# Optimization experiments

Hardware: AMD Instinct MI355X
Metric: run time of the kernel (lower is better)

## Reference

```python
import jax, jax.numpy as jnp
import numpy as np

N_NODES = 50000
N_EDGES = 300000
D_NODE = 128
D_EDGE = 128
D_HID = 256
D_OUT = 128


def setup_inputs() -> dict:
    key = jax.random.key(0)
    k1, k2, k3, k4, k5, k6, k7 = jax.random.split(key, 7)
    node_attr = jax.random.normal(k1, (N_NODES, D_NODE), dtype=jnp.float32)
    edge_contact_attr = jax.random.normal(k2, (N_EDGES, D_EDGE), dtype=jnp.float32)
    edge_contact_index = jax.random.randint(k3, (2, N_EDGES), 0, N_NODES, dtype=jnp.int32)
    d_in = 2 * D_NODE + D_EDGE  # 384: [sender, receiver, edge] concat
    W1 = jax.random.normal(k4, (d_in, D_HID), dtype=jnp.float32) / jnp.sqrt(jnp.float32(d_in))
    b1 = jnp.zeros((D_HID,), dtype=jnp.float32)
    W2 = jax.random.normal(k5, (D_HID, D_OUT), dtype=jnp.float32) / jnp.sqrt(jnp.float32(D_HID))
    b2 = jnp.zeros((D_OUT,), dtype=jnp.float32)
    ln_gamma = jnp.ones((D_OUT,), dtype=jnp.float32)
    ln_beta = jnp.zeros((D_OUT,), dtype=jnp.float32)
    return {
        "node_attr": node_attr,
        "edge_contact_attr": edge_contact_attr,
        "edge_contact_index": edge_contact_index,
        "W1": W1, "b1": b1, "W2": W2, "b2": b2,
        "ln_gamma": ln_gamma, "ln_beta": ln_beta,
    }


def _layer_norm(x, gamma, beta, eps=1e-5):
    mu = jnp.mean(x, axis=-1, keepdims=True)
    var = jnp.var(x, axis=-1, keepdims=True)
    return (x - mu) * jax.lax.rsqrt(var + eps) * gamma + beta


def reference(node_attr, edge_contact_attr, edge_contact_index,
              W1, b1, W2, b2, ln_gamma, ln_beta):
    senders_idx = edge_contact_index[0]
    receivers_idx = edge_contact_index[1]
    senders_attr = node_attr[senders_idx]      # [E, D_NODE] gather
    receivers_attr = node_attr[receivers_idx]  # [E, D_NODE] gather
    edge_messages = jnp.concatenate(
        [senders_attr, receivers_attr, edge_contact_attr], axis=1)  # [E, 384]
    h = jax.nn.relu(edge_messages @ W1 + b1)   # [E, D_HID]
    h = h @ W2 + b2                            # [E, D_OUT]
    new_edge_contact_attr = _layer_norm(h, ln_gamma, ln_beta)
    return new_edge_contact_attr
```

## Files before the change

### kernel.cpp

```cpp
#include <hip/hip_runtime.h>

#define E_TOT   300000
#define DN      128
#define DOUT    128

typedef float  f32x4  __attribute__((ext_vector_type(4)));
typedef __bf16 bf16x8 __attribute__((ext_vector_type(8)));

__device__ __forceinline__ unsigned short f2bf(float f) {
    union { float f; unsigned int u; } v; v.f = f;
    return (unsigned short)((v.u + 0x7FFFu + ((v.u >> 16) & 1u)) >> 16);
}

__global__ void prep_weights(const float* __restrict__ W1,
                             const float* __restrict__ W2,
                             unsigned short* __restrict__ W1p,
                             unsigned short* __restrict__ W2p) {
    int t = blockIdx.x * 256 + threadIdx.x;
    if (t < 384 * 256) {
        int k = t >> 8, n = t & 255;
        W1p[(((k >> 6) << 8) + n) * 64 + (k & 63)] = f2bf(W1[t]);
    } else {
        int t2 = t - 384 * 256;
        int k = t2 >> 7, n = t2 & 127;
        W2p[(((k >> 6) << 7) + n) * 64 + (k & 63)] = f2bf(W2[t2]);
    }
}

__global__ __launch_bounds__(256, 3) void edge_mlp(
    const float* __restrict__ node_attr,
    const float* __restrict__ edge_attr,
    const int*   __restrict__ eidx,
    const unsigned short* __restrict__ W1p,
    const unsigned short* __restrict__ W2p,
    const float* __restrict__ b1,
    const float* __restrict__ b2,
    const float* __restrict__ ln_g,
    const float* __restrict__ ln_b,
    float* __restrict__ out)
{
    __shared__ __align__(16) unsigned short smem[26112];
    __shared__ int sIdx[64], rIdx[64];

    unsigned short* Xc   = smem;
    unsigned short* W1c  = smem + 4608;
    unsigned short* hbuf = smem;
    unsigned short* W2c  = smem + 16896;

    const int tid  = threadIdx.x;
    const int wid  = tid >> 6;
    const int lane = tid & 63;
    const int quad = lane >> 4;
    const int l16  = lane & 15;
    const int eb   = blockIdx.x * 64;

    if (tid < 128) {
        int r = tid & 63;
        int e = eb + r; if (e >= E_TOT) e = E_TOT - 1;
        if (tid < 64) sIdx[r] = eidx[e];
        else          rIdx[r] = eidx[E_TOT + e];
    }

    f32x4 acc[4][4];
    #pragma unroll
    for (int i = 0; i < 4; ++i)
        #pragma unroll
        for (int j = 0; j < 4; ++j)
            acc[i][j] = (f32x4){0.f, 0.f, 0.f, 0.f};

    __syncthreads();

    #pragma unroll 1
    for (int c = 0; c < 6; ++c) {
        if (c) __syncthreads();
        const int coloff = (c & 1) << 6;
        #pragma unroll
        for (int i = 0; i < 4; ++i) {
            int id  = (i << 8) + tid;
            int row = id >> 4;
            int q4  = id & 15;
            const float* src;
            if (c < 2)      src = node_attr + (size_t)sIdx[row] * DN;
            else if (c < 4) src = node_attr + (size_t)rIdx[row] * DN;
            else {
                int e = eb + row; if (e >= E_TOT) e = E_TOT - 1;
                src = edge_attr + (size_t)e * DN;
            }
            float4 v = *(const float4*)(src + coloff + (q4 << 2));
            ushort4 p;
            p.x = f2bf(v.x); p.y = f2bf(v.y); p.z = f2bf(v.z); p.w = f2bf(v.w);
            *(ushort4*)(Xc + row * 72 + (q4 << 2)) = p;
        }
        const unsigned short* wsrc = W1p + c * (256 * 64);
        #pragma unroll
        for (int i = 0; i < 8; ++i) {
            int id = (i << 8) + tid;
            *(uint4*)(W1c + (id >> 3) * 72 + ((id & 7) << 3)) =
                *(const uint4*)(wsrc + (id << 3));
        }
        __syncthreads();
        #pragma unroll
        for (int ks = 0; ks < 2; ++ks) {
            bf16x8 a[4];
            #pragma unroll
            for (int mt = 0; mt < 4; ++mt)
                a[mt] = *(const bf16x8*)(Xc + ((mt << 4) + l16) * 72 + (ks << 5) + (quad << 3));
            #pragma unroll
            for (int nt = 0; nt < 4; ++nt) {
                bf16x8 b = *(const bf16x8*)(W1c + ((wid << 6) + (nt << 4) + l16) * 72 + (ks << 5) + (quad << 3));
                #pragma unroll
                for (int mt = 0; mt < 4; ++mt)
                    acc[mt][nt] = __builtin_amdgcn_mfma_f32_16x16x32_bf16(a[mt], b, acc[mt][nt], 0, 0, 0);
            }
        }
    }

    float b1v[4];
    #pragma unroll
    for (int nt = 0; nt < 4; ++nt) b1v[nt] = b1[(wid << 6) + (nt << 4) + l16];
    __syncthreads();
    #pragma unroll
    for (int mt = 0; mt < 4; ++mt)
        #pragma unroll
        for (int nt = 0; nt < 4; ++nt)
            #pragma unroll
            for (int r = 0; r < 4; ++r) {
                int row = (mt << 4) + (quad << 2) + r;
                int col = (wid << 6) + (nt << 4) + l16;
                float v = acc[mt][nt][r] + b1v[nt];
                hbuf[row * 264 + col] = f2bf(v > 0.f ? v : 0.f);
            }
    __syncthreads();

    f32x4 acc2[8];
    #pragma unroll
    for (int nt = 0; nt < 8; ++nt) acc2[nt] = (f32x4){0.f, 0.f, 0.f, 0.f};

    #pragma unroll 1
    for (int c2 = 0; c2 < 4; ++c2) {
        if (c2) __syncthreads();
        const unsigned short* wsrc = W2p + c2 * (128 * 64);
        #pragma unroll
        for (int i = 0; i < 4; ++i) {
            int id = (i << 8) + tid;
            *(uint4*)(W2c + (id >> 3) * 72 + ((id & 7) << 3)) =
                *(const uint4*)(wsrc + (id << 3));
        }
        __syncthreads();
        #pragma unroll
        for (int ks = 0; ks < 2; ++ks) {
            bf16x8 a = *(const bf16x8*)(hbuf + ((wid << 4) + l16) * 264 + (c2 << 6) + (ks << 5) + (quad << 3));
            #pragma unroll
            for (int nt = 0; nt < 8; ++nt) {
                bf16x8 b = *(const bf16x8*)(W2c + ((nt << 4) + l16) * 72 + (ks << 5) + (quad << 3));
                acc2[nt] = __builtin_amdgcn_mfma_f32_16x16x32_bf16(a, b, acc2[nt], 0, 0, 0);
            }
        }
    }

    float b2v[8], gv[8], bev[8];
    #pragma unroll
    for (int nt = 0; nt < 8; ++nt) {
        int n = (nt << 4) + l16;
        b2v[nt] = b2[n]; gv[nt] = ln_g[n]; bev[nt] = ln_b[n];
    }
    #pragma unroll
    for (int r = 0; r < 4; ++r) {
        int e = eb + (wid << 4) + (quad << 2) + r;
        float x[8];
        float s = 0.f, s2 = 0.f;
        #pragma unroll
        for (int nt = 0; nt < 8; ++nt) {
            x[nt] = acc2[nt][r] + b2v[nt];
            s += x[nt]; s2 += x[nt] * x[nt];
        }
        #pragma unroll
        for (int m = 1; m < 16; m <<= 1) {
            s  += __shfl_xor(s, m, 64);
            s2 += __shfl_xor(s2, m, 64);
        }
        const float mu  = s * (1.f / 128.f);
        const float var = s2 * (1.f / 128.f) - mu * mu;
        const float rs  = rsqrtf(var + 1e-5f);
        if (e < E_TOT) {
            float* orow = out + (size_t)e * DOUT;
            #pragma unroll
            for (int nt = 0; nt < 8; ++nt)
                orow[(nt << 4) + l16] = (x[nt] - mu) * rs * gv[nt] + bev[nt];
        }
    }
}

extern "C" void kernel_launch(void* const* d_in, const int* in_sizes, int n_in,
                              void* d_out, int out_size, void* d_ws, size_t ws_size,
                              hipStream_t stream) {
    const float* node_attr = (const float*)d_in[0];
    const float* edge_attr = (const float*)d_in[1];
    const int*   eidx      = (const int*)d_in[2];
    const float* W1        = (const float*)d_in[3];
    const float* b1        = (const float*)d_in[4];
    const float* W2        = (const float*)d_in[5];
    const float* b2        = (const float*)d_in[6];
    const float* ln_g      = (const float*)d_in[7];
    const float* ln_b      = (const float*)d_in[8];

    unsigned short* W1p = (unsigned short*)d_ws;
    unsigned short* W2p = W1p + 384 * 256;

    prep_weights<<<512, 256, 0, stream>>>(W1, W2, W1p, W2p);

    const int nblocks = (E_TOT + 63) / 64;
    edge_mlp<<<nblocks, 256, 0, stream>>>(node_attr, edge_attr, eidx,
                                          W1p, W2p, b1, b2, ln_g, ln_b,
                                          (float*)d_out);
}
```

Measured before the change: 418.2 us.

## Load MFMA fragments directly from global memory, bypassing LDS staging

Gathered node and edge features are now loaded from global memory straight into per-lane registers in MFMA A-fragment layout and converted with the packed bf16 conversion instruction. W1 and W2 fragments are also read directly from the pre-packed global buffers instead of being staged through shared memory. This removes most LDS traffic and the per-chunk barriers, and shrinks shared memory to the hidden buffer, which may allow higher occupancy. In exchange each wave re-reads weight data from global/L2 independently, and the activation loads are less coalesced (32-byte pieces per lane).

```diff
diff --git a/kernel.cpp b/kernel.cpp
--- a/kernel.cpp
+++ b/kernel.cpp
@@ -6,10 +6,26 @@
 
 typedef float  f32x4  __attribute__((ext_vector_type(4)));
 typedef __bf16 bf16x8 __attribute__((ext_vector_type(8)));
+typedef unsigned int u32;
 
 __device__ __forceinline__ unsigned short f2bf(float f) {
     union { float f; unsigned int u; } v; v.f = f;
     return (unsigned short)((v.u + 0x7FFFu + ((v.u >> 16) & 1u)) >> 16);
+}
+
+__device__ __forceinline__ u32 cvt_pk_bf16(float lo, float hi) {
+    u32 r;
+    asm("v_cvt_pk_bf16_f32 %0, %1, %2" : "=v"(r) : "v"(lo), "v"(hi));
+    return r;
+}
+
+__device__ __forceinline__ bf16x8 make_frag(float4 u0, float4 u1) {
+    union { u32 w[4]; bf16x8 v; } r;
+    r.w[0] = cvt_pk_bf16(u0.x, u0.y);
+    r.w[1] = cvt_pk_bf16(u0.z, u0.w);
+    r.w[2] = cvt_pk_bf16(u1.x, u1.y);
+    r.w[3] = cvt_pk_bf16(u1.z, u1.w);
+    return r.v;
 }
 
 __global__ void prep_weights(const float* __restrict__ W1,
@@ -39,13 +55,7 @@
     const float* __restrict__ ln_b,
     float* __restrict__ out)
 {
-    __shared__ __align__(16) unsigned short smem[26112];
-    __shared__ int sIdx[64], rIdx[64];
-
-    unsigned short* Xc   = smem;
-    unsigned short* W1c  = smem + 4608;
-    unsigned short* hbuf = smem;
-    unsigned short* W2c  = smem + 16896;
+    __shared__ __align__(16) unsigned short hbuf[64 * 264];
 
     const int tid  = threadIdx.x;
     const int wid  = tid >> 6;
@@ -54,11 +64,14 @@
     const int l16  = lane & 15;
     const int eb   = blockIdx.x * 64;
 
-    if (tid < 128) {
-        int r = tid & 63;
-        int e = eb + r; if (e >= E_TOT) e = E_TOT - 1;
-        if (tid < 64) sIdx[r] = eidx[e];
-        else          rIdx[r] = eidx[E_TOT + e];
+    u32 offS[4], offR[4], offE[4];
+    #pragma unroll
+    for (int mt = 0; mt < 4; ++mt) {
+        int e = eb + (mt << 4) + l16;
+        if (e >= E_TOT) e = E_TOT - 1;
+        offS[mt] = (u32)eidx[e] * (DN * 4);
+        offR[mt] = (u32)eidx[E_TOT + e] * (DN * 4);
+        offE[mt] = (u32)e * (DN * 4);
     }
 
     f32x4 acc[4][4];
@@ -68,49 +81,33 @@
         for (int j = 0; j < 4; ++j)
             acc[i][j] = (f32x4){0.f, 0.f, 0.f, 0.f};
 
-    __syncthreads();
-
+    const int fbase = ((0) << 6);
+    (void)fbase;
     #pragma unroll 1
     for (int c = 0; c < 6; ++c) {
-        if (c) __syncthreads();
-        const int coloff = (c & 1) << 6;
-        #pragma unroll
-        for (int i = 0; i < 4; ++i) {
-            int id  = (i << 8) + tid;
-            int row = id >> 4;
-            int q4  = id & 15;
-            const float* src;
-            if (c < 2)      src = node_attr + (size_t)sIdx[row] * DN;
-            else if (c < 4) src = node_attr + (size_t)rIdx[row] * DN;
-            else {
-                int e = eb + row; if (e >= E_TOT) e = E_TOT - 1;
-                src = edge_attr + (size_t)e * DN;
-            }
-            float4 v = *(const float4*)(src + coloff + (q4 << 2));
-            ushort4 p;
-            p.x = f2bf(v.x); p.y = f2bf(v.y); p.z = f2bf(v.z); p.w = f2bf(v.w);
-            *(ushort4*)(Xc + row * 72 + (q4 << 2)) = p;
-        }
-        const unsigned short* wsrc = W1p + c * (256 * 64);
-        #pragma unroll
-        for (int i = 0; i < 8; ++i) {
-            int id = (i << 8) + tid;
-            *(uint4*)(W1c + (id >> 3) * 72 + ((id & 7) << 3)) =
-                *(const uint4*)(wsrc + (id << 3));
-        }
-        __syncthreads();
+        const int f0 = ((c & 1) << 6) + (quad << 3);
+        bf16x8 a[2][4];
+        #pragma unroll
+        for (int mt = 0; mt < 4; ++mt) {
+            u32 off = (c < 2) ? offS[mt] : (c < 4) ? offR[mt] : offE[mt];
+            const char* basep = (const char*)((c < 4) ? node_attr : edge_attr);
+            const float* s = (const float*)(basep + off);
+            float4 u0 = *(const float4*)(s + f0);
+            float4 u1 = *(const float4*)(s + f0 + 4);
+            float4 v0 = *(const float4*)(s + f0 + 32);
+            float4 v1 = *(const float4*)(s + f0 + 36);
+            a[0][mt] = make_frag(u0, u1);
+            a[1][mt] = make_frag(v0, v1);
+        }
+        const unsigned short* wbase = W1p + (((c << 8) + (wid << 6)) << 6);
         #pragma unroll
         for (int ks = 0; ks < 2; ++ks) {
-            bf16x8 a[4];
-            #pragma unroll
-            for (int mt = 0; mt < 4; ++mt)
-                a[mt] = *(const bf16x8*)(Xc + ((mt << 4) + l16) * 72 + (ks << 5) + (quad << 3));
             #pragma unroll
             for (int nt = 0; nt < 4; ++nt) {
-                bf16x8 b = *(const bf16x8*)(W1c + ((wid << 6) + (nt << 4) + l16) * 72 + (ks << 5) + (quad << 3));
+                bf16x8 b = *(const bf16x8*)(wbase + (((nt << 4) + l16) << 6) + (ks << 5) + (quad << 3));
                 #pragma unroll
                 for (int mt = 0; mt < 4; ++mt)
-                    acc[mt][nt] = __builtin_amdgcn_mfma_f32_16x16x32_bf16(a[mt], b, acc[mt][nt], 0, 0, 0);
+                    acc[mt][nt] = __builtin_amdgcn_mfma_f32_16x16x32_bf16(a[ks][mt], b, acc[mt][nt], 0, 0, 0);
             }
         }
     }
@@ -118,7 +115,6 @@
     float b1v[4];
     #pragma unroll
     for (int nt = 0; nt < 4; ++nt) b1v[nt] = b1[(wid << 6) + (nt << 4) + l16];
-    __syncthreads();
     #pragma unroll
     for (int mt = 0; mt < 4; ++mt)
         #pragma unroll
@@ -138,21 +134,13 @@
 
     #pragma unroll 1
     for (int c2 = 0; c2 < 4; ++c2) {
-        if (c2) __syncthreads();
-        const unsigned short* wsrc = W2p + c2 * (128 * 64);
-        #pragma unroll
-        for (int i = 0; i < 4; ++i) {
-            int id = (i << 8) + tid;
-            *(uint4*)(W2c + (id >> 3) * 72 + ((id & 7) << 3)) =
-                *(const uint4*)(wsrc + (id << 3));
-        }
-        __syncthreads();
+        const unsigned short* w2base = W2p + ((c2 << 7) << 6);
         #pragma unroll
         for (int ks = 0; ks < 2; ++ks) {
             bf16x8 a = *(const bf16x8*)(hbuf + ((wid << 4) + l16) * 264 + (c2 << 6) + (ks << 5) + (quad << 3));
             #pragma unroll
             for (int nt = 0; nt < 8; ++nt) {
-                bf16x8 b = *(const bf16x8*)(W2c + ((nt << 4) + l16) * 72 + (ks << 5) + (quad << 3));
+                bf16x8 b = *(const bf16x8*)(w2base + (((nt << 4) + l16) << 6) + (ks << 5) + (quad << 3));
                 acc2[nt] = __builtin_amdgcn_mfma_f32_16x16x32_bf16(a, b, acc2[nt], 0, 0, 0);
             }
         }
```

After: 667.6 us. 59.6% more time.
